# Optimization experiments

Measured on AMD Instinct MI355X. Metric: run time of the kernel, lower is better.

Reference implementation:

```python
import jax, jax.numpy as jnp
import numpy as np

N = 2_000_000   # points
C = 65_536      # cluster centers
F = 8           # point feature dim
D = 3           # coord dim


def _dense_params(key, din, dout):
    kw, kb = jax.random.split(key)
    scale = jnp.sqrt(2.0 / din).astype(jnp.float32)
    return (jax.random.normal(kw, (din, dout), jnp.float32) * scale,
            jnp.zeros((dout,), jnp.float32))


def setup_inputs() -> dict:
    key = jax.random.key(0)
    ks = jax.random.split(key, 16)
    inp = {
        "point_features": jax.random.normal(ks[0], (N, F), jnp.float32),
        "labels": jax.random.randint(ks[1], (N,), 0, C, jnp.int32),
        "cluster_centers": jax.random.normal(ks[2], (C, D), jnp.float32),
        "points": jax.random.normal(ks[3], (N, D), jnp.float32),
    }
    # edge MLP: (F+D)->8->16->32->64
    dims = [F + D, 8, 16, 32, 64]
    for i in range(4):
        w, b = _dense_params(ks[4 + i], dims[i], dims[i + 1])
        inp[f"we{i}"] = w
        inp[f"be{i}"] = b
    # attention MLP: (F+D)->64->1
    inp["wa0"], inp["ba0"] = _dense_params(ks[8], F + D, 64)
    inp["wa1"], inp["ba1"] = _dense_params(ks[9], 64, 1)
    # output MLP: 64->128->256
    inp["wo0"], inp["bo0"] = _dense_params(ks[10], 64, 128)
    inp["wo1"], inp["bo1"] = _dense_params(ks[11], 128, 256)
    return inp


def reference(point_features, labels, cluster_centers, points,
              we0, be0, we1, be1, we2, be2, we3, be3,
              wa0, ba0, wa1, ba1, wo0, bo0, wo1, bo1):
    relu = jax.nn.relu
    # gather center coords for each point, build edge input [N, F+D]
    center_coords = cluster_centers[labels]
    x = jnp.concatenate([point_features, center_coords - points], axis=-1)
    # edge MLP 8->16->32->64 (all relu)
    h = relu(x @ we0 + be0)
    h = relu(h @ we1 + be1)
    h = relu(h @ we2 + be2)
    h = relu(h @ we3 + be3)            # [N, 64]
    # attention MLP 64->1 sigmoid
    a = relu(x @ wa0 + ba0)
    a = jax.nn.sigmoid(a @ wa1 + ba1)  # [N, 1]
    t = h * a
    # scatter-sum into clusters
    agg = jax.ops.segment_sum(t, labels, num_segments=C)  # [C, 64]
    # output MLP 128->256 (relu, relu)
    o = relu(agg @ wo0 + bo0)
    o = relu(o @ wo1 + bo1)            # [C, 256]
    return o
```

## Files before the change

### kernel.cpp

```cpp
#include <hip/hip_runtime.h>
#include <hip/hip_bf16.h>
#include <math.h>
#include <stdint.h>

#define TPB 256
#define NCB 32

__global__ __launch_bounds__(TPB) void hist_kernel(
    const int* __restrict__ labels, int* __restrict__ counts, int n)
{
    int i = blockIdx.x * TPB + threadIdx.x;
    if (i < n) atomicAdd(&counts[labels[i]], 1);
}

__global__ __launch_bounds__(256) void scan_local(
    const int* __restrict__ counts, int* __restrict__ off,
    int* __restrict__ bsum, int C)
{
    __shared__ int sh[256];
    int t = threadIdx.x;
    int i = blockIdx.x * 256 + t;
    int v = (i < C) ? counts[i] : 0;
    sh[t] = v;
    __syncthreads();
    for (int d = 1; d < 256; d <<= 1) {
        int u = (t >= d) ? sh[t - d] : 0;
        __syncthreads();
        sh[t] += u;
        __syncthreads();
    }
    if (i < C) off[i] = sh[t] - v;
    if (t == 255) bsum[blockIdx.x] = sh[255];
}

__global__ __launch_bounds__(256) void scan_base(
    int* __restrict__ bsum, int* __restrict__ off, int nb, int C)
{
    __shared__ int sh[256];
    int t = threadIdx.x;
    int v = (t < nb) ? bsum[t] : 0;
    sh[t] = v;
    __syncthreads();
    for (int d = 1; d < 256; d <<= 1) {
        int u = (t >= d) ? sh[t - d] : 0;
        __syncthreads();
        sh[t] += u;
        __syncthreads();
    }
    if (t < nb) bsum[t] = sh[t] - v;
    if (t == 255) off[C] = sh[255];
}

__global__ __launch_bounds__(256) void scan_apply(
    int* __restrict__ off, int* __restrict__ cursor,
    const int* __restrict__ bsum, int C)
{
    int i = blockIdx.x * 256 + threadIdx.x;
    if (i < C) {
        int v = off[i] + bsum[blockIdx.x];
        off[i] = v;
        cursor[i] = v;
    }
}

__global__ __launch_bounds__(TPB, 4) void point_mlp_kernel(
    const float* __restrict__ pf, const int* __restrict__ labels,
    const float* __restrict__ centers, const float* __restrict__ points,
    const float* __restrict__ we0, const float* __restrict__ be0,
    const float* __restrict__ we1, const float* __restrict__ be1,
    const float* __restrict__ we2, const float* __restrict__ be2,
    const float* __restrict__ we3, const float* __restrict__ be3,
    const float* __restrict__ wa0, const float* __restrict__ ba0,
    const float* __restrict__ wa1, const float* __restrict__ ba1,
    int* __restrict__ cursor, unsigned short* __restrict__ tsort, int n)
{
    int i = blockIdx.x * TPB + threadIdx.x;
    if (i >= n) return;

    float x[11];
    const float4* pf4 = (const float4*)pf;
    float4 p0 = pf4[(size_t)i * 2 + 0];
    float4 p1 = pf4[(size_t)i * 2 + 1];
    x[0] = p0.x; x[1] = p0.y; x[2] = p0.z; x[3] = p0.w;
    x[4] = p1.x; x[5] = p1.y; x[6] = p1.z; x[7] = p1.w;

    int lbl = labels[i];
    x[8]  = centers[lbl * 3 + 0] - points[(size_t)i * 3 + 0];
    x[9]  = centers[lbl * 3 + 1] - points[(size_t)i * 3 + 1];
    x[10] = centers[lbl * 3 + 2] - points[(size_t)i * 3 + 2];

    int pos = atomicAdd(&cursor[lbl], 1);

    float s = ba1[0];
#pragma unroll
    for (int j = 0; j < 64; j++) {
        float aj = ba0[j];
#pragma unroll
        for (int k = 0; k < 11; k++) aj = fmaf(x[k], wa0[k * 64 + j], aj);
        aj = fmaxf(aj, 0.f);
        s = fmaf(aj, wa1[j], s);
    }
    float gate = 1.f / (1.f + __expf(-s));

    float h1[8];
#pragma unroll
    for (int j = 0; j < 8; j++) {
        float v = be0[j];
#pragma unroll
        for (int k = 0; k < 11; k++) v = fmaf(x[k], we0[k * 8 + j], v);
        h1[j] = fmaxf(v, 0.f);
    }
    float h2[16];
#pragma unroll
    for (int j = 0; j < 16; j++) {
        float v = be1[j];
#pragma unroll
        for (int k = 0; k < 8; k++) v = fmaf(h1[k], we1[k * 16 + j], v);
        h2[j] = fmaxf(v, 0.f);
    }
    float h3[32];
#pragma unroll
    for (int j = 0; j < 32; j++) {
        float v = be2[j];
#pragma unroll
        for (int k = 0; k < 16; k++) v = fmaf(h2[k], we2[k * 32 + j], v);
        h3[j] = fmaxf(v, 0.f);
    }

    uint4* dst = (uint4*)(tsort + (size_t)pos * 64);
#pragma unroll
    for (int g = 0; g < 8; g++) {
        unsigned int w[4];
#pragma unroll
        for (int q = 0; q < 4; q++) {
            unsigned int packed = 0;
#pragma unroll
            for (int h = 0; h < 2; h++) {
                int j = g * 8 + q * 2 + h;
                float v = be3[j];
#pragma unroll
                for (int k = 0; k < 32; k++) v = fmaf(h3[k], we3[k * 64 + j], v);
                v = fmaxf(v, 0.f) * gate;
                __hip_bfloat16 b = __float2bfloat16(v);
                unsigned short us = *(unsigned short*)&b;
                packed |= ((unsigned int)us) << (16 * h);
            }
            w[q] = packed;
        }
        dst[g] = make_uint4(w[0], w[1], w[2], w[3]);
    }
}

__global__ __launch_bounds__(TPB) void agg_outmlp_kernel(
    const unsigned short* __restrict__ tsort,
    const int* __restrict__ off,
    const float* __restrict__ wo0, const float* __restrict__ bo0,
    const float* __restrict__ wo1, const float* __restrict__ bo1,
    float* __restrict__ out)
{
    __shared__ float s_agg[NCB * 64];
    __shared__ float s_mid[NCB * 128];
    int tid = threadIdx.x;
    int c0 = blockIdx.x * NCB;

    {
        int lane  = tid & 63;
        int w     = tid >> 6;
        int rlane = lane >> 3;
        int word  = lane & 7;
        const uint4* t128 = (const uint4*)tsort;
#define BF_LO(u) (__uint_as_float((u) << 16))
#define BF_HI(u) (__uint_as_float((u) & 0xffff0000u))
        for (int lc = w * 8; lc < w * 8 + 8; lc++) {
            int rb = off[c0 + lc];
            int re = off[c0 + lc + 1];
            float a[8];
#pragma unroll
            for (int q = 0; q < 8; q++) a[q] = 0.f;
            for (int r = rb; r < re; r += 16) {
                int r0 = r + rlane;
                int r1 = r + 8 + rlane;
                uint4 v0 = make_uint4(0u, 0u, 0u, 0u);
                uint4 v1 = make_uint4(0u, 0u, 0u, 0u);
                if (r0 < re) v0 = t128[(size_t)r0 * 8 + word];
                if (r1 < re) v1 = t128[(size_t)r1 * 8 + word];
                a[0] += BF_LO(v0.x) + BF_LO(v1.x);
                a[1] += BF_HI(v0.x) + BF_HI(v1.x);
                a[2] += BF_LO(v0.y) + BF_LO(v1.y);
                a[3] += BF_HI(v0.y) + BF_HI(v1.y);
                a[4] += BF_LO(v0.z) + BF_LO(v1.z);
                a[5] += BF_HI(v0.z) + BF_HI(v1.z);
                a[6] += BF_LO(v0.w) + BF_LO(v1.w);
                a[7] += BF_HI(v0.w) + BF_HI(v1.w);
            }
#pragma unroll
            for (int m = 8; m < 64; m <<= 1) {
#pragma unroll
                for (int q = 0; q < 8; q++) a[q] += __shfl_xor(a[q], m, 64);
            }
            if (rlane == 0) {
                *(float4*)&s_agg[lc * 64 + word * 8 + 0] =
                    make_float4(a[0], a[1], a[2], a[3]);
                *(float4*)&s_agg[lc * 64 + word * 8 + 4] =
                    make_float4(a[4], a[5], a[6], a[7]);
            }
        }
#undef BF_LO
#undef BF_HI
    }
    __syncthreads();

    {
        int j = tid & 127;
        int g = tid >> 7;
        float acc[16];
        float b = bo0[j];
#pragma unroll
        for (int c = 0; c < 16; c++) acc[c] = b;
        for (int k = 0; k < 64; k += 4) {
            float w0 = wo0[(k + 0) * 128 + j];
            float w1 = wo0[(k + 1) * 128 + j];
            float w2 = wo0[(k + 2) * 128 + j];
            float w3 = wo0[(k + 3) * 128 + j];
#pragma unroll
            for (int c = 0; c < 16; c++) {
                const float4 av = *(const float4*)&s_agg[(g * 16 + c) * 64 + k];
                acc[c] = fmaf(av.x, w0, acc[c]);
                acc[c] = fmaf(av.y, w1, acc[c]);
                acc[c] = fmaf(av.z, w2, acc[c]);
                acc[c] = fmaf(av.w, w3, acc[c]);
            }
        }
#pragma unroll
        for (int c = 0; c < 16; c++)
            s_mid[(g * 16 + c) * 128 + j] = fmaxf(acc[c], 0.f);
    }
    __syncthreads();

    {
        int m = tid;
        float acc[NCB];
        float b = bo1[m];
#pragma unroll
        for (int c = 0; c < NCB; c++) acc[c] = b;
        for (int j = 0; j < 128; j += 4) {
            float w0 = wo1[(j + 0) * 256 + m];
            float w1 = wo1[(j + 1) * 256 + m];
            float w2 = wo1[(j + 2) * 256 + m];
            float w3 = wo1[(j + 3) * 256 + m];
#pragma unroll
            for (int c = 0; c < NCB; c++) {
                const float4 mv = *(const float4*)&s_mid[c * 128 + j];
                acc[c] = fmaf(mv.x, w0, acc[c]);
                acc[c] = fmaf(mv.y, w1, acc[c]);
                acc[c] = fmaf(mv.z, w2, acc[c]);
                acc[c] = fmaf(mv.w, w3, acc[c]);
            }
        }
#pragma unroll
        for (int c = 0; c < NCB; c++)
            out[(size_t)(c0 + c) * 256 + m] = fmaxf(acc[c], 0.f);
    }
}

extern "C" void kernel_launch(void* const* d_in, const int* in_sizes, int n_in,
                              void* d_out, int out_size, void* d_ws, size_t ws_size,
                              hipStream_t stream)
{
    const float* pf      = (const float*)d_in[0];
    const int*   labels  = (const int*)d_in[1];
    const float* centers = (const float*)d_in[2];
    const float* points  = (const float*)d_in[3];
    const float* we0 = (const float*)d_in[4];
    const float* be0 = (const float*)d_in[5];
    const float* we1 = (const float*)d_in[6];
    const float* be1 = (const float*)d_in[7];
    const float* we2 = (const float*)d_in[8];
    const float* be2 = (const float*)d_in[9];
    const float* we3 = (const float*)d_in[10];
    const float* be3 = (const float*)d_in[11];
    const float* wa0 = (const float*)d_in[12];
    const float* ba0 = (const float*)d_in[13];
    const float* wa1 = (const float*)d_in[14];
    const float* ba1 = (const float*)d_in[15];
    const float* wo0 = (const float*)d_in[16];
    const float* bo0 = (const float*)d_in[17];
    const float* wo1 = (const float*)d_in[18];
    const float* bo1 = (const float*)d_in[19];
    float* out = (float*)d_out;

    int n = in_sizes[0] / 8;
    int C = in_sizes[2] / 3;

    int* counts = (int*)d_ws;
    int* cursor = counts + C;
    int* off    = cursor + C;
    int* bsum   = off + C + 1;
    uintptr_t tb = ((uintptr_t)(bsum + 256) + 255) & ~(uintptr_t)255;
    unsigned short* tsort = (unsigned short*)tb;

    hipMemsetAsync(counts, 0, (size_t)C * sizeof(int), stream);

    int pblocks = (n + TPB - 1) / TPB;
    int nb = (C + 255) / 256;
    hist_kernel<<<pblocks, TPB, 0, stream>>>(labels, counts, n);
    scan_local<<<nb, 256, 0, stream>>>(counts, off, bsum, C);
    scan_base<<<1, 256, 0, stream>>>(bsum, off, nb, C);
    scan_apply<<<nb, 256, 0, stream>>>(off, cursor, bsum, C);

    point_mlp_kernel<<<pblocks, TPB, 0, stream>>>(
        pf, labels, centers, points,
        we0, be0, we1, be1, we2, be2, we3, be3,
        wa0, ba0, wa1, ba1, cursor, tsort, n);

    agg_outmlp_kernel<<<C / NCB, TPB, 0, stream>>>(
        tsort, off, wo0, bo0, wo1, bo1, out);
}
```

Before: 603.2 us.

## Register-tile output MLP GEMMs with 8-wide column tiles and padded LDS rows

Restructures the two small output-MLP matmuls in the aggregation kernel so each thread computes a 2x8 or 4x8 register tile. Weights load as float4 from global memory and activations as float4 from LDS. The LDS row strides are padded (68/132) to avoid bank conflicts on the strided row reads. Weight loads per FMA drop sharply and output stores become vectorized, at the cost of less coalesced per-lane weight access and different register pressure.

```diff
diff --git a/kernel.cpp b/kernel.cpp
--- a/kernel.cpp
+++ b/kernel.cpp
@@ -5,6 +5,8 @@
 
 #define TPB 256
 #define NCB 32
+#define SAGG_LD 68
+#define SMID_LD 132
 
 __global__ __launch_bounds__(TPB) void hist_kernel(
     const int* __restrict__ labels, int* __restrict__ counts, int n)
@@ -158,8 +160,8 @@
     const float* __restrict__ wo1, const float* __restrict__ bo1,
     float* __restrict__ out)
 {
-    __shared__ float s_agg[NCB * 64];
-    __shared__ float s_mid[NCB * 128];
+    __shared__ float s_agg[NCB * SAGG_LD];
+    __shared__ float s_mid[NCB * SMID_LD];
     int tid = threadIdx.x;
     int c0 = blockIdx.x * NCB;
 
@@ -199,9 +201,9 @@
                 for (int q = 0; q < 8; q++) a[q] += __shfl_xor(a[q], m, 64);
             }
             if (rlane == 0) {
-                *(float4*)&s_agg[lc * 64 + word * 8 + 0] =
+                *(float4*)&s_agg[lc * SAGG_LD + word * 8 + 0] =
                     make_float4(a[0], a[1], a[2], a[3]);
-                *(float4*)&s_agg[lc * 64 + word * 8 + 4] =
+                *(float4*)&s_agg[lc * SAGG_LD + word * 8 + 4] =
                     make_float4(a[4], a[5], a[6], a[7]);
             }
         }
@@ -211,55 +213,93 @@
     __syncthreads();
 
     {
-        int j = tid & 127;
-        int g = tid >> 7;
-        float acc[16];
-        float b = bo0[j];
-#pragma unroll
-        for (int c = 0; c < 16; c++) acc[c] = b;
+        int mg = tid & 15;
+        int cg = tid >> 4;
+        int m0 = mg * 8;
+        float acc[2][8];
+#pragma unroll
+        for (int mi = 0; mi < 8; mi++) {
+            float b = bo0[m0 + mi];
+            acc[0][mi] = b;
+            acc[1][mi] = b;
+        }
         for (int k = 0; k < 64; k += 4) {
-            float w0 = wo0[(k + 0) * 128 + j];
-            float w1 = wo0[(k + 1) * 128 + j];
-            float w2 = wo0[(k + 2) * 128 + j];
-            float w3 = wo0[(k + 3) * 128 + j];
-#pragma unroll
-            for (int c = 0; c < 16; c++) {
-                const float4 av = *(const float4*)&s_agg[(g * 16 + c) * 64 + k];
-                acc[c] = fmaf(av.x, w0, acc[c]);
-                acc[c] = fmaf(av.y, w1, acc[c]);
-                acc[c] = fmaf(av.z, w2, acc[c]);
-                acc[c] = fmaf(av.w, w3, acc[c]);
-            }
-        }
-#pragma unroll
-        for (int c = 0; c < 16; c++)
-            s_mid[(g * 16 + c) * 128 + j] = fmaxf(acc[c], 0.f);
+            float4 a0 = *(const float4*)&s_agg[(cg * 2 + 0) * SAGG_LD + k];
+            float4 a1 = *(const float4*)&s_agg[(cg * 2 + 1) * SAGG_LD + k];
+            float av0[4] = {a0.x, a0.y, a0.z, a0.w};
+            float av1[4] = {a1.x, a1.y, a1.z, a1.w};
+#pragma unroll
+            for (int q = 0; q < 4; q++) {
+                float4 wlo = *(const float4*)&wo0[(k + q) * 128 + m0];
+                float4 whi = *(const float4*)&wo0[(k + q) * 128 + m0 + 4];
+                float wv[8] = {wlo.x, wlo.y, wlo.z, wlo.w,
+                               whi.x, whi.y, whi.z, whi.w};
+#pragma unroll
+                for (int mi = 0; mi < 8; mi++) {
+                    acc[0][mi] = fmaf(av0[q], wv[mi], acc[0][mi]);
+                    acc[1][mi] = fmaf(av1[q], wv[mi], acc[1][mi]);
+                }
+            }
+        }
+#pragma unroll
+        for (int c = 0; c < 2; c++) {
+            float4 lo = make_float4(fmaxf(acc[c][0], 0.f), fmaxf(acc[c][1], 0.f),
+                                    fmaxf(acc[c][2], 0.f), fmaxf(acc[c][3], 0.f));
+            float4 hi = make_float4(fmaxf(acc[c][4], 0.f), fmaxf(acc[c][5], 0.f),
+                                    fmaxf(acc[c][6], 0.f), fmaxf(acc[c][7], 0.f));
+            *(float4*)&s_mid[(cg * 2 + c) * SMID_LD + m0 + 0] = lo;
+            *(float4*)&s_mid[(cg * 2 + c) * SMID_LD + m0 + 4] = hi;
+        }
     }
     __syncthreads();
 
     {
-        int m = tid;
-        float acc[NCB];
-        float b = bo1[m];
-#pragma unroll
-        for (int c = 0; c < NCB; c++) acc[c] = b;
+        int mg = tid & 31;
+        int cg = tid >> 5;
+        int m0 = mg * 8;
+        float acc[4][8];
+#pragma unroll
+        for (int mi = 0; mi < 8; mi++) {
+            float b = bo1[m0 + mi];
+            acc[0][mi] = b;
+            acc[1][mi] = b;
+            acc[2][mi] = b;
+            acc[3][mi] = b;
+        }
         for (int j = 0; j < 128; j += 4) {
-            float w0 = wo1[(j + 0) * 256 + m];
-            float w1 = wo1[(j + 1) * 256 + m];
-            float w2 = wo1[(j + 2) * 256 + m];
-            float w3 = wo1[(j + 3) * 256 + m];
-#pragma unroll
-            for (int c = 0; c < NCB; c++) {
-                const float4 mv = *(const float4*)&s_mid[c * 128 + j];
-                acc[c] = fmaf(mv.x, w0, acc[c]);
-                acc[c] = fmaf(mv.y, w1, acc[c]);
-                acc[c] = fmaf(mv.z, w2, acc[c]);
-                acc[c] = fmaf(mv.w, w3, acc[c]);
-            }
-        }
-#pragma unroll
-        for (int c = 0; c < NCB; c++)
-            out[(size_t)(c0 + c) * 256 + m] = fmaxf(acc[c], 0.f);
+            float4 a0 = *(const float4*)&s_mid[(cg * 4 + 0) * SMID_LD + j];
+            float4 a1 = *(const float4*)&s_mid[(cg * 4 + 1) * SMID_LD + j];
+            float4 a2 = *(const float4*)&s_mid[(cg * 4 + 2) * SMID_LD + j];
+            float4 a3 = *(const float4*)&s_mid[(cg * 4 + 3) * SMID_LD + j];
+            float av0[4] = {a0.x, a0.y, a0.z, a0.w};
+            float av1[4] = {a1.x, a1.y, a1.z, a1.w};
+            float av2[4] = {a2.x, a2.y, a2.z, a2.w};
+            float av3[4] = {a3.x, a3.y, a3.z, a3.w};
+#pragma unroll
+            for (int q = 0; q < 4; q++) {
+                float4 wlo = *(const float4*)&wo1[(j + q) * 256 + m0];
+                float4 whi = *(const float4*)&wo1[(j + q) * 256 + m0 + 4];
+                float wv[8] = {wlo.x, wlo.y, wlo.z, wlo.w,
+                               whi.x, whi.y, whi.z, whi.w};
+#pragma unroll
+                for (int mi = 0; mi < 8; mi++) {
+                    acc[0][mi] = fmaf(av0[q], wv[mi], acc[0][mi]);
+                    acc[1][mi] = fmaf(av1[q], wv[mi], acc[1][mi]);
+                    acc[2][mi] = fmaf(av2[q], wv[mi], acc[2][mi]);
+                    acc[3][mi] = fmaf(av3[q], wv[mi], acc[3][mi]);
+                }
+            }
+        }
+#pragma unroll
+        for (int c = 0; c < 4; c++) {
+            float4 lo = make_float4(fmaxf(acc[c][0], 0.f), fmaxf(acc[c][1], 0.f),
+                                    fmaxf(acc[c][2], 0.f), fmaxf(acc[c][3], 0.f));
+            float4 hi = make_float4(fmaxf(acc[c][4], 0.f), fmaxf(acc[c][5], 0.f),
+                                    fmaxf(acc[c][6], 0.f), fmaxf(acc[c][7], 0.f));
+            size_t row = (size_t)(c0 + cg * 4 + c) * 256 + m0;
+            *(float4*)&out[row + 0] = lo;
+            *(float4*)&out[row + 4] = hi;
+        }
     }
 }
 
```

Result: no change. 597.0 us (-1.0%).
